# Kernel tuning notes

Hardware: AMD Instinct MI355X
Metric: run time of the kernel (lower is better)

The kernel has to match this reference:

```python
import jax, jax.numpy as jnp
import numpy as np

N_NODES = 200000
N_EDGES = 1000000
N_Q = 64
N_REL_ROWS = 401  # 2*n_rel + 1
D = 128
A = 64


def setup_inputs() -> dict:
    key = jax.random.key(0)
    ks = jax.random.split(key, 16)
    s = 0.05  # param scale
    return {
        'hidden': jax.random.normal(ks[0], (N_NODES, D), jnp.float32),
        'q_emb': jax.random.normal(ks[1], (N_Q, D), jnp.float32),
        'rela_embed': jax.random.normal(ks[2], (N_REL_ROWS, D), jnp.float32),
        'Ws_w': jax.random.normal(ks[3], (A, D), jnp.float32) * s,
        'Ws_b': jax.random.normal(ks[4], (A,), jnp.float32) * s,
        'Wr_w': jax.random.normal(ks[5], (A, D), jnp.float32) * s,
        'Wq_w': jax.random.normal(ks[6], (A, D), jnp.float32) * s,
        'Wqr_w': jax.random.normal(ks[7], (A, D), jnp.float32) * s,
        'walpha_w': jax.random.normal(ks[8], (1, A), jnp.float32) * s,
        'walpha_b': jax.random.normal(ks[9], (1,), jnp.float32) * s,
        'Wh_w': jax.random.normal(ks[10], (D, D), jnp.float32) * s,
        'r_idx': jax.random.randint(ks[11], (N_EDGES,), 0, N_Q, jnp.int32),
        'rel': jax.random.randint(ks[12], (N_EDGES,), 0, N_REL_ROWS, jnp.int32),
        'sub': jax.random.randint(ks[13], (N_EDGES,), 0, N_NODES, jnp.int32),
        'obj': jax.random.randint(ks[14], (N_EDGES,), 0, N_NODES, jnp.int32),
    }


def reference(hidden, q_emb, rela_embed, Ws_w, Ws_b, Wr_w, Wq_w, Wqr_w,
              walpha_w, walpha_b, Wh_w, r_idx, rel, sub, obj):
    # Gather per-edge features (memory-bound irregular access)
    hs = hidden[sub]          # [E, D]
    hr = rela_embed[rel]      # [E, D]
    h_qr = q_emb[r_idx]       # [E, D]

    # Fused small attention MLP: sigmoid(w_alpha(relu(Ws hs + Wr hr + Wq hq + Wqr (hr*hq))))
    pre = (jnp.einsum('ed,ad->ea', hs, Ws_w) + Ws_b
           + jnp.einsum('ed,ad->ea', hr, Wr_w)
           + jnp.einsum('ed,ad->ea', h_qr, Wq_w)
           + jnp.einsum('ed,ad->ea', hr * h_qr, Wqr_w))  # [E, A]
    alpha = jax.nn.sigmoid(jnp.einsum('ea,oa->eo', jax.nn.relu(pre), walpha_w) + walpha_b)  # [E, 1]

    # Gated message + scatter-sum aggregation per target node
    message = alpha * (hs * hr)                                   # [E, D]
    message_agg = jax.ops.segment_sum(message, obj, num_segments=N_NODES)  # [N, D]

    hidden_new = jax.nn.relu(jnp.einsum('nd,od->no', message_agg, Wh_w))   # [N, D]
    return hidden_new, alpha
```

## Files before the change

### kernel.cpp

```cpp
#include <hip/hip_runtime.h>
#include <hip/hip_bf16.h>
#include <hip/hip_fp8.h>

#define N_NODES 200000
#define N_EDGES 1000000
#define NQ 64
#define NRELR 401
#define DIM 128
#define AA 64
#define NBK 3125
#define CAP 512

typedef __attribute__((ext_vector_type(8))) short short8_t;
typedef __attribute__((ext_vector_type(4))) float f32x4;

static __device__ inline short f2bs(float f) {
  __hip_bfloat16 h = __float2bfloat16(f);
  return __builtin_bit_cast(short, h);
}
static __device__ inline float bs2f(unsigned short u) {
  unsigned x = ((unsigned)u) << 16;
  return __builtin_bit_cast(float, x);
}
static __device__ inline unsigned pk2(float lo, float hi) {
  unsigned short a = (unsigned short)__builtin_bit_cast(short, __float2bfloat16(lo));
  unsigned short b = (unsigned short)__builtin_bit_cast(short, __float2bfloat16(hi));
  return (unsigned)a | ((unsigned)b << 16);
}
static __device__ inline unsigned char f2e4(float f) {
  __hip_fp8_e4m3 h(f);
  return (unsigned char)h.__x;
}
static __device__ inline float e42f(unsigned char b) {
  __hip_fp8_e4m3 h;
  h.__x = (__hip_fp8_storage_t)b;
  return (float)h;
}
static __device__ inline void atomic_pk_bf16_s(unsigned voff, unsigned val,
                                               const unsigned short* base) {
  asm volatile("global_atomic_pk_add_bf16 %0, %1, %2"
               :: "v"(voff), "v"(val), "s"((unsigned long long)base) : "memory");
}
static __device__ inline short8_t pack8(float4 a, float4 b) {
  short8_t v;
  v[0] = f2bs(a.x); v[1] = f2bs(a.y); v[2] = f2bs(a.z); v[3] = f2bs(a.w);
  v[4] = f2bs(b.x); v[5] = f2bs(b.y); v[6] = f2bs(b.z); v[7] = f2bs(b.w);
  return v;
}

#define CBK 401
#define SBK 512
#define HBK 64
__global__ __launch_bounds__(256) void prep_kernel(
    const float* __restrict__ hidden, const float* __restrict__ qemb,
    const float* __restrict__ rela, const float* __restrict__ Ws,
    const float* __restrict__ Wsb, const float* __restrict__ Wr,
    const float* __restrict__ Wq, const float* __restrict__ Wqr,
    const int* __restrict__ obj,
    unsigned char* __restrict__ C8, unsigned char* __restrict__ S8,
    unsigned short* __restrict__ relab, short* __restrict__ hidb,
    int* __restrict__ cnt) {
  int b = blockIdx.x;
  int t = threadIdx.x;

  if (b < CBK) {
    __shared__ __hip_bfloat16 hqs[64][136];
    __shared__ __hip_bfloat16 vts[128][72];
    __shared__ float hr_f[128];
    __shared__ float trp[4][64];
    __shared__ float tr_s[64];
    int rho = b;

    if (t < 128) {
      float hv = rela[rho * DIM + t];
      hr_f[t] = hv;
      relab[rho * DIM + t] = (unsigned short)f2bs(hv);
    }
    __syncthreads();
    for (int i = t; i < 64 * 128; i += 256) {
      int q = i >> 7, d = i & 127;
      hqs[q][d] = __float2bfloat16(qemb[i]);
      int a = i >> 7;
      vts[d][a] = __float2bfloat16(Wq[i] + hr_f[d] * Wqr[i]);
    }
    {
      int a = t & 63, qt = t >> 6;
      const float* wr = Wr + a * DIM + qt * 32;
      float p = 0.f;
#pragma unroll 8
      for (int i = 0; i < 32; ++i) p += wr[i] * hr_f[qt * 32 + i];
      trp[qt][a] = p;
    }
    __syncthreads();
    if (t < 64)
      tr_s[t] = trp[0][t] + trp[1][t] + trp[2][t] + trp[3][t] + Wsb[t];
    __syncthreads();

    int qg = t >> 4, ag = t & 15;
    int q0 = qg * 4, a0 = ag * 4;
    float acc[4][4];
#pragma unroll
    for (int i = 0; i < 4; ++i)
#pragma unroll
      for (int j = 0; j < 4; ++j) acc[i][j] = 0.f;
    for (int d = 0; d < DIM; ++d) {
      float hv[4], wv[4];
#pragma unroll
      for (int i = 0; i < 4; ++i) hv[i] = __bfloat162float(hqs[q0 + i][d]);
#pragma unroll
      for (int j = 0; j < 4; ++j) wv[j] = __bfloat162float(vts[d][a0 + j]);
#pragma unroll
      for (int i = 0; i < 4; ++i)
#pragma unroll
        for (int j = 0; j < 4; ++j) acc[i][j] += hv[i] * wv[j];
    }
#pragma unroll
    for (int i = 0; i < 4; ++i)
#pragma unroll
      for (int j = 0; j < 4; ++j) {
        int q = q0 + i, a = a0 + j;
        C8[((size_t)rho * 64 + q) * 64 + a] = f2e4(acc[i][j] + tr_s[a]);
      }
  } else if (b < CBK + SBK) {
    int lane = t & 63;
    int lr = lane & 15, lg = lane >> 4;
    int gw = (b - CBK) * 4 + (t >> 6);
    const int NWV = SBK * 4;

    short8_t bf[4][4];
#pragma unroll
    for (int ot = 0; ot < 4; ++ot)
#pragma unroll
      for (int kt = 0; kt < 4; ++kt) {
        const float* wp = Ws + (size_t)(ot * 16 + lr) * DIM + kt * 32 + lg * 8;
        bf[ot][kt] = pack8(*(const float4*)wp, *(const float4*)(wp + 4));
      }

    for (int tt = gw; tt < N_NODES / 16; tt += NWV) {
      const float* ap = hidden + (size_t)tt * 16 * DIM + (size_t)lr * DIM;
      short8_t a[4];
#pragma unroll
      for (int kt = 0; kt < 4; ++kt) {
        const float* p = ap + kt * 32 + lg * 8;
        a[kt] = pack8(*(const float4*)p, *(const float4*)(p + 4));
        *(short8_t*)(hidb + ((size_t)tt * 16 + lr) * DIM + kt * 32 + lg * 8) = a[kt];
      }
      f32x4 acc[4];
#pragma unroll
      for (int ot = 0; ot < 4; ++ot) {
        acc[ot] = (f32x4){0.f, 0.f, 0.f, 0.f};
#pragma unroll
        for (int kt = 0; kt < 4; ++kt)
          acc[ot] = __builtin_amdgcn_mfma_f32_16x16x32_bf16(a[kt], bf[ot][kt], acc[ot], 0, 0, 0);
      }
#pragma unroll
      for (int ot = 0; ot < 4; ++ot)
#pragma unroll
        for (int r = 0; r < 4; ++r)
          S8[((size_t)tt * 16 + lg * 4 + r) * 64 + ot * 16 + lr] = f2e4(acc[ot][r]);
    }
  } else {
    __shared__ int h[NBK];
    int z = b - CBK - SBK;
    for (int i = t; i < NBK; i += 256) h[i] = 0;
    __syncthreads();
    for (int e = z * 256 + t; e < N_EDGES; e += HBK * 256)
      atomicAdd(&h[obj[e] >> 6], 1);
    __syncthreads();
    for (int i = t; i < NBK; i += 256)
      if (h[i]) atomicAdd(&cnt[i], h[i]);
  }
}

__global__ __launch_bounds__(256) void scan_kernel(
    const int* __restrict__ cnt, int* __restrict__ base, int* __restrict__ cur) {
  __shared__ int part[256];
  int t = threadIdx.x;
  const int PER = (NBK + 255) / 256;
  int lo = t * PER;
  int loc[PER];
  int s = 0;
#pragma unroll
  for (int k = 0; k < PER; ++k) {
    loc[k] = s;
    int idx = lo + k;
    s += (idx < NBK) ? cnt[idx] : 0;
  }
  part[t] = s;
  __syncthreads();
  for (int off = 1; off < 256; off <<= 1) {
    int v = (t >= off) ? part[t - off] : 0;
    __syncthreads();
    part[t] += v;
    __syncthreads();
  }
  int pre = (t == 0) ? 0 : part[t - 1];
#pragma unroll
  for (int k = 0; k < PER; ++k) {
    int idx = lo + k;
    if (idx < NBK) {
      base[idx] = pre + loc[k];
      cur[idx] = pre + loc[k];
    }
  }
  if (t == 255) base[NBK] = part[255];
}

__global__ __launch_bounds__(256) void scatter2_kernel(
    const int* __restrict__ ridx, const int* __restrict__ rel,
    const int* __restrict__ sub, const int* __restrict__ obj,
    int* __restrict__ cur, uint2* __restrict__ recs) {
  __shared__ int h[NBK];
  __shared__ int loff[NBK];
  __shared__ int lcur[NBK];
  int t = threadIdx.x, z = blockIdx.x;
  for (int i = t; i < NBK; i += 256) { h[i] = 0; lcur[i] = 0; }
  __syncthreads();
  for (int e = z * 256 + t; e < N_EDGES; e += HBK * 256)
    atomicAdd(&h[obj[e] >> 6], 1);
  __syncthreads();
  for (int i = t; i < NBK; i += 256)
    if (h[i]) loff[i] = atomicAdd(&cur[i], h[i]);
  __syncthreads();
  for (int e = z * 256 + t; e < N_EDGES; e += HBK * 256) {
    int s = sub[e], r = rel[e], q = ridx[e], o = obj[e];
    int bb = o >> 6;
    int rq = r * 64 + q;
    int p = loff[bb] + atomicAdd(&lcur[bb], 1);
    uint2 rc;
    rc.x = (unsigned)s | ((unsigned)(o & 63) << 18) | ((unsigned)(rq & 0xFF) << 24);
    rc.y = (unsigned)(rq >> 8) | ((unsigned)e << 7);
    recs[p] = rc;
  }
}

__global__ __launch_bounds__(256) void bucket2_kernel(
    const unsigned* __restrict__ hid32, const unsigned* __restrict__ rel32,
    const unsigned char* __restrict__ S8, const unsigned char* __restrict__ C8,
    const float* __restrict__ wal, const float* __restrict__ walb,
    const int* __restrict__ base, const uint2* __restrict__ recs,
    unsigned* __restrict__ agg32, float* __restrict__ alpha_out) {
  __shared__ uint2 lrec[CAP];
  __shared__ unsigned short ord[CAP];
  __shared__ int cnt2[64];
  __shared__ int scn[65];
  __shared__ int curs[64];
  int t = threadIdx.x, b = blockIdx.x;
  int lane = t & 63, w = t >> 6;
  int lo = base[b], hi = base[b + 1];
  int cnt = hi - lo;
  int nbase = b * 64;
  float wa = wal[lane];
  float wb = walb[0];

  if (t < 64) cnt2[t] = 0;
  __syncthreads();

  if (cnt <= CAP) {
    for (int i = t; i < cnt; i += 256) {
      uint2 rc = recs[lo + i];
      lrec[i] = rc;
      atomicAdd(&cnt2[(rc.x >> 18) & 63], 1);
    }
    __syncthreads();
    if (t < 64) scn[t + 1] = cnt2[t];
    if (t == 0) scn[0] = 0;
    __syncthreads();
    for (int off = 1; off < 64; off <<= 1) {
      int v = 0;
      if (t < 64) { v = scn[t + 1]; if (t + 1 > off) v += scn[t + 1 - off]; }
      __syncthreads();
      if (t < 64) scn[t + 1] = v;
      __syncthreads();
    }
    if (t < 64) curs[t] = scn[t];
    __syncthreads();
    for (int i = t; i < cnt; i += 256) {
      int oin = (lrec[i].x >> 18) & 63;
      int p = atomicAdd(&curs[oin], 1);
      ord[p] = (unsigned short)i;
    }
    __syncthreads();

    int n0 = w * 16;
    int s0 = scn[n0], s1 = scn[n0 + 16];
    float m0 = 0.f, m1 = 0.f;
    int curn = -1;
    for (int j = s0; j < s1; j += 4) {
      int nv = s1 - j;
      if (nv > 4) nv = 4;
      int sdx[4], on[4], rq[4], ei[4];
      float y[4], h0[4], h1[4], g0[4], g1[4];
#pragma unroll
      for (int u = 0; u < 4; ++u) {
        int idx = (u < nv) ? (j + u) : j;
        uint2 rc = lrec[ord[idx]];
        unsigned rx = __builtin_amdgcn_readfirstlane(rc.x);
        unsigned ry = __builtin_amdgcn_readfirstlane(rc.y);
        sdx[u] = rx & 0x3FFFF;
        on[u] = (rx >> 18) & 63;
        rq[u] = ((rx >> 24) & 0xFF) | ((ry & 0x7F) << 8);
        ei[u] = ry >> 7;
      }
#pragma unroll
      for (int u = 0; u < 4; ++u) {
        float x = e42f(S8[(size_t)sdx[u] * 64 + lane]) +
                  e42f(C8[(size_t)rq[u] * 64 + lane]);
        y[u] = fmaxf(x, 0.f) * wa;
      }
#pragma unroll
      for (int u = 0; u < 4; ++u) {
        unsigned hp = hid32[(size_t)sdx[u] * 64 + lane];
        unsigned rp = rel32[(size_t)(rq[u] >> 6) * 64 + lane];
        h0[u] = bs2f((unsigned short)(hp & 0xffff));
        h1[u] = bs2f((unsigned short)(hp >> 16));
        g0[u] = bs2f((unsigned short)(rp & 0xffff));
        g1[u] = bs2f((unsigned short)(rp >> 16));
      }
#pragma unroll
      for (int off = 32; off; off >>= 1) {
#pragma unroll
        for (int u = 0; u < 4; ++u) y[u] += __shfl_xor(y[u], off);
      }
#pragma unroll
      for (int u = 0; u < 4; ++u) {
        if (u < nv) {
          float al = 1.f / (1.f + __expf(-(y[u] + wb)));
          if (on[u] != curn) {
            if (curn >= 0)
              agg32[(size_t)(nbase + curn) * 64 + lane] = pk2(m0, m1);
            curn = on[u];
            m0 = 0.f; m1 = 0.f;
          }
          m0 += al * h0[u] * g0[u];
          m1 += al * h1[u] * g1[u];
          if (lane == 0) alpha_out[ei[u]] = al;
        }
      }
    }
    if (curn >= 0)
      agg32[(size_t)(nbase + curn) * 64 + lane] = pk2(m0, m1);
    for (int n = n0; n < n0 + 16; ++n) {
      if (cnt2[n] == 0)
        agg32[(size_t)(nbase + n) * 64 + lane] = 0u;
    }
  } else {
    for (int n = w; n < 64; n += 4)
      agg32[(size_t)(nbase + n) * 64 + lane] = 0u;
    __syncthreads();
    unsigned voff = (unsigned)lane * 4;
    for (int i = lo + w * 4; i < hi; i += 16) {
      int nv = hi - i;
      if (nv > 4) nv = 4;
      for (int u = 0; u < 4; ++u) {
        if (u >= nv) break;
        uint2 rc = recs[i + u];
        unsigned rx = __builtin_amdgcn_readfirstlane(rc.x);
        unsigned ry = __builtin_amdgcn_readfirstlane(rc.y);
        int sdx = rx & 0x3FFFF;
        int on = (rx >> 18) & 63;
        int rq = ((rx >> 24) & 0xFF) | ((ry & 0x7F) << 8);
        int ei = ry >> 7;
        float x = e42f(S8[(size_t)sdx * 64 + lane]) + e42f(C8[(size_t)rq * 64 + lane]);
        float y = fmaxf(x, 0.f) * wa;
        for (int off = 32; off; off >>= 1) y += __shfl_xor(y, off);
        float al = 1.f / (1.f + __expf(-(y + wb)));
        unsigned hp = hid32[(size_t)sdx * 64 + lane];
        unsigned rp = rel32[(size_t)(rq >> 6) * 64 + lane];
        float v0 = al * bs2f((unsigned short)(hp & 0xffff)) * bs2f((unsigned short)(rp & 0xffff));
        float v1 = al * bs2f((unsigned short)(hp >> 16)) * bs2f((unsigned short)(rp >> 16));
        atomic_pk_bf16_s(voff, pk2(v0, v1), (const unsigned short*)(agg32 + (size_t)(nbase + on) * 64));
        if (lane == 0) alpha_out[ei] = al;
      }
    }
  }
}

__global__ __launch_bounds__(256) void out_gemm_bf(
    const float* __restrict__ Wh, const short* __restrict__ aggb,
    float* __restrict__ out) {
  int lane = threadIdx.x & 63;
  int lr = lane & 15, lg = lane >> 4;
  int gw = (blockIdx.x * blockDim.x + threadIdx.x) >> 6;
  int nwv = (gridDim.x * blockDim.x) >> 6;

  short8_t b[8][4];
#pragma unroll
  for (int ot = 0; ot < 8; ++ot)
#pragma unroll
    for (int kt = 0; kt < 4; ++kt) {
      const float* wp = Wh + (size_t)(ot * 16 + lr) * DIM + kt * 32 + lg * 8;
      b[ot][kt] = pack8(*(const float4*)wp, *(const float4*)(wp + 4));
    }

  for (int t = gw; t < N_NODES / 16; t += nwv) {
    const short* ap = aggb + ((size_t)t * 16 + lr) * DIM;
    short8_t a[4];
#pragma unroll
    for (int kt = 0; kt < 4; ++kt)
      a[kt] = *(const short8_t*)(ap + kt * 32 + lg * 8);
    f32x4 acc[8];
#pragma unroll
    for (int ot = 0; ot < 8; ++ot) {
      acc[ot] = (f32x4){0.f, 0.f, 0.f, 0.f};
#pragma unroll
      for (int kt = 0; kt < 4; ++kt)
        acc[ot] = __builtin_amdgcn_mfma_f32_16x16x32_bf16(a[kt], b[ot][kt], acc[ot], 0, 0, 0);
    }
    float* op = out + (size_t)t * 16 * DIM;
#pragma unroll
    for (int ot = 0; ot < 8; ++ot)
#pragma unroll
      for (int r = 0; r < 4; ++r)
        op[(size_t)(lg * 4 + r) * DIM + ot * 16 + lr] = fmaxf(acc[ot][r], 0.f);
  }
}

__global__ __launch_bounds__(256) void tq_kernel(
    const float* __restrict__ qemb, const float* __restrict__ Wq,
    float* __restrict__ Tq) {
  int t = blockIdx.x * 256 + threadIdx.x;
  if (t >= NQ * AA) return;
  int q = t >> 6, a = t & 63;
  float s = 0.f;
#pragma unroll 4
  for (int d = 0; d < DIM; ++d) s += qemb[q * DIM + d] * Wq[a * DIM + d];
  Tq[t] = s;
}

__global__ __launch_bounds__(256) void build_C_old(
    const float* __restrict__ qemb, const float* __restrict__ rela,
    const float* __restrict__ Wr, const float* __restrict__ Wqr,
    const float* __restrict__ Wsb, const float* __restrict__ Tq,
    __hip_bfloat16* __restrict__ Cout) {
  __shared__ float hrq[64 * 129];
  __shared__ float wqrT[128 * 65];
  __shared__ float wrT[128 * 65];
  __shared__ float hr_s[128];
  __shared__ float tr_s[64];
  int rho = blockIdx.x;
  int t = threadIdx.x;
  if (t < 128) hr_s[t] = rela[rho * DIM + t];
  __syncthreads();
  for (int i = t; i < 64 * 128; i += 256) {
    int a = i >> 7, d = i & 127;
    hrq[a * 129 + d] = qemb[i] * hr_s[d];
    wqrT[d * 65 + a] = Wqr[i];
    wrT[d * 65 + a] = Wr[i];
  }
  __syncthreads();
  if (t < 64) {
    float s = 0.f;
#pragma unroll 4
    for (int d = 0; d < DIM; ++d) s += wrT[d * 65 + t] * hr_s[d];
    tr_s[t] = s + Wsb[t];
  }
  __syncthreads();
  int qg = t >> 4, ag = t & 15;
  int q0 = qg * 4, a0 = ag * 4;
  float acc[4][4];
#pragma unroll
  for (int i = 0; i < 4; ++i)
#pragma unroll
    for (int j = 0; j < 4; ++j) acc[i][j] = 0.f;
  for (int d = 0; d < DIM; ++d) {
    float hv[4], wv[4];
#pragma unroll
    for (int i = 0; i < 4; ++i) hv[i] = hrq[(q0 + i) * 129 + d];
#pragma unroll
    for (int j = 0; j < 4; ++j) wv[j] = wqrT[d * 65 + a0 + j];
#pragma unroll
    for (int i = 0; i < 4; ++i)
#pragma unroll
      for (int j = 0; j < 4; ++j) acc[i][j] += hv[i] * wv[j];
  }
#pragma unroll
  for (int i = 0; i < 4; ++i)
#pragma unroll
    for (int j = 0; j < 4; ++j) {
      int q = q0 + i, a = a0 + j;
      Cout[(rho * 64 + q) * 64 + a] = __float2bfloat16(acc[i][j] + Tq[q * 64 + a] + tr_s[a]);
    }
}

__global__ __launch_bounds__(256) void build_S_old(
    const float* __restrict__ hidden, const float* __restrict__ Ws,
    __hip_bfloat16* __restrict__ Sout) {
  int lane = threadIdx.x & 63;
  int lr = lane & 15, lg = lane >> 4;
  int gw = (blockIdx.x * blockDim.x + threadIdx.x) >> 6;
  int nwv = (gridDim.x * blockDim.x) >> 6;
  short8_t b[4][4];
#pragma unroll
  for (int ot = 0; ot < 4; ++ot)
#pragma unroll
    for (int kt = 0; kt < 4; ++kt) {
      const float* wp = Ws + (size_t)(ot * 16 + lr) * DIM + kt * 32 + lg * 8;
      b[ot][kt] = pack8(*(const float4*)wp, *(const float4*)(wp + 4));
    }
  for (int t = gw; t < N_NODES / 16; t += nwv) {
    const float* ap = hidden + (size_t)t * 16 * DIM + (size_t)lr * DIM;
    short8_t a[4];
#pragma unroll
    for (int kt = 0; kt < 4; ++kt) {
      const float* p = ap + kt * 32 + lg * 8;
      a[kt] = pack8(*(const float4*)p, *(const float4*)(p + 4));
    }
    f32x4 acc[4];
#pragma unroll
    for (int ot = 0; ot < 4; ++ot) {
      acc[ot] = (f32x4){0.f, 0.f, 0.f, 0.f};
#pragma unroll
      for (int kt = 0; kt < 4; ++kt)
        acc[ot] = __builtin_amdgcn_mfma_f32_16x16x32_bf16(a[kt], b[ot][kt], acc[ot], 0, 0, 0);
    }
#pragma unroll
    for (int ot = 0; ot < 4; ++ot)
#pragma unroll
      for (int r = 0; r < 4; ++r)
        Sout[((size_t)t * 16 + lg * 4 + r) * 64 + ot * 16 + lr] = __float2bfloat16(acc[ot][r]);
  }
}

__global__ __launch_bounds__(256) void edge_kernel_old(
    const float* __restrict__ hidden, const float* __restrict__ rela,
    const __hip_bfloat16* __restrict__ S, const __hip_bfloat16* __restrict__ C,
    const float* __restrict__ wal, const float* __restrict__ walb,
    const int* __restrict__ ridx, const int* __restrict__ rel,
    const int* __restrict__ sub, const int* __restrict__ obj,
    float* __restrict__ agg, float* __restrict__ alpha_out) {
  int lane = threadIdx.x & 63;
  int wid = (blockIdx.x * blockDim.x + threadIdx.x) >> 6;
  const int CH = 124;
  int e0 = wid * CH;
  if (e0 >= N_EDGES) return;
  int e1 = e0 + CH;
  if (e1 > N_EDGES) e1 = N_EDGES;
  float wa = wal[lane];
  float wb = walb[0];
  for (int e = e0; e < e1; e += 4) {
    int4 ss = *(const int4*)(sub + e);
    int4 rr = *(const int4*)(rel + e);
    int4 qq = *(const int4*)(ridx + e);
    int4 oo = *(const int4*)(obj + e);
    int s[4] = {ss.x, ss.y, ss.z, ss.w};
    int r[4] = {rr.x, rr.y, rr.z, rr.w};
    int q[4] = {qq.x, qq.y, qq.z, qq.w};
    int o[4] = {oo.x, oo.y, oo.z, oo.w};
    float y[4];
#pragma unroll
    for (int u = 0; u < 4; ++u) {
      float x = __bfloat162float(S[(size_t)s[u] * 64 + lane]) +
                __bfloat162float(C[((size_t)r[u] * 64 + q[u]) * 64 + lane]);
      y[u] = fmaxf(x, 0.f) * wa;
    }
    float h0[4], h1[4], r0[4], r1[4];
#pragma unroll
    for (int u = 0; u < 4; ++u) {
      h0[u] = hidden[(size_t)s[u] * DIM + lane];
      h1[u] = hidden[(size_t)s[u] * DIM + 64 + lane];
      r0[u] = rela[(size_t)r[u] * DIM + lane];
      r1[u] = rela[(size_t)r[u] * DIM + 64 + lane];
    }
#pragma unroll
    for (int off = 32; off; off >>= 1) {
#pragma unroll
      for (int u = 0; u < 4; ++u) y[u] += __shfl_xor(y[u], off);
    }
    float al[4];
#pragma unroll
    for (int u = 0; u < 4; ++u) al[u] = 1.f / (1.f + __expf(-(y[u] + wb)));
#pragma unroll
    for (int u = 0; u < 4; ++u) {
      unsafeAtomicAdd(&agg[(size_t)o[u] * DIM + lane], al[u] * h0[u] * r0[u]);
      unsafeAtomicAdd(&agg[(size_t)o[u] * DIM + 64 + lane], al[u] * h1[u] * r1[u]);
    }
    if (lane == 0)
      *(float4*)(alpha_out + e) = make_float4(al[0], al[1], al[2], al[3]);
  }
}

__global__ __launch_bounds__(256) void out_gemm_old(
    const float* __restrict__ Wh, float* __restrict__ agg) {
  int lane = threadIdx.x & 63;
  int lr = lane & 15, lg = lane >> 4;
  int gw = (blockIdx.x * blockDim.x + threadIdx.x) >> 6;
  int nwv = (gridDim.x * blockDim.x) >> 6;
  short8_t b[8][4];
#pragma unroll
  for (int ot = 0; ot < 8; ++ot)
#pragma unroll
    for (int kt = 0; kt < 4; ++kt) {
      const float* wp = Wh + (size_t)(ot * 16 + lr) * DIM + kt * 32 + lg * 8;
      b[ot][kt] = pack8(*(const float4*)wp, *(const float4*)(wp + 4));
    }
  for (int t = gw; t < N_NODES / 16; t += nwv) {
    float* ap = agg + (size_t)t * 16 * DIM + (size_t)lr * DIM;
    short8_t a[4];
#pragma unroll
    for (int kt = 0; kt < 4; ++kt) {
      const float* p = ap + kt * 32 + lg * 8;
      a[kt] = pack8(*(const float4*)p, *(const float4*)(p + 4));
    }
    f32x4 acc[8];
#pragma unroll
    for (int ot = 0; ot < 8; ++ot) {
      acc[ot] = (f32x4){0.f, 0.f, 0.f, 0.f};
#pragma unroll
      for (int kt = 0; kt < 4; ++kt)
        acc[ot] = __builtin_amdgcn_mfma_f32_16x16x32_bf16(a[kt], b[ot][kt], acc[ot], 0, 0, 0);
    }
    float* op = agg + (size_t)t * 16 * DIM;
#pragma unroll
    for (int ot = 0; ot < 8; ++ot)
#pragma unroll
      for (int r = 0; r < 4; ++r)
        op[(size_t)(lg * 4 + r) * DIM + ot * 16 + lr] = fmaxf(acc[ot][r], 0.f);
  }
}

extern "C" void kernel_launch(void* const* d_in, const int* in_sizes, int n_in,
                              void* d_out, int out_size, void* d_ws, size_t ws_size,
                              hipStream_t stream) {
  const float* hidden = (const float*)d_in[0];
  const float* qemb   = (const float*)d_in[1];
  const float* rela   = (const float*)d_in[2];
  const float* Ws_w   = (const float*)d_in[3];
  const float* Ws_b   = (const float*)d_in[4];
  const float* Wr_w   = (const float*)d_in[5];
  const float* Wq_w   = (const float*)d_in[6];
  const float* Wqr_w  = (const float*)d_in[7];
  const float* wal_w  = (const float*)d_in[8];
  const float* wal_b  = (const float*)d_in[9];
  const float* Wh_w   = (const float*)d_in[10];
  const int* r_idx    = (const int*)d_in[11];
  const int* rel      = (const int*)d_in[12];
  const int* sub      = (const int*)d_in[13];
  const int* obj      = (const int*)d_in[14];

  float* out_hidden = (float*)d_out;
  float* out_alpha  = out_hidden + (size_t)N_NODES * DIM;

  char* ws = (char*)d_ws;
  const size_t OFF_C8  = 0;
  const size_t SZ_C8   = (size_t)NRELR * 64 * 64;
  const size_t OFF_S8  = OFF_C8 + SZ_C8;
  const size_t SZ_S8   = (size_t)N_NODES * 64;
  const size_t OFF_RB  = OFF_S8 + SZ_S8;
  const size_t SZ_RB   = (size_t)NRELR * DIM * 2;
  const size_t OFF_HB  = OFF_RB + SZ_RB;
  const size_t SZ_HB   = (size_t)N_NODES * DIM * 2;
  const size_t OFF_AG  = OFF_HB + SZ_HB;
  const size_t OFF_CNT = OFF_AG + SZ_HB;
  const size_t OFF_BASE= OFF_CNT + 16384;
  const size_t OFF_CUR = OFF_BASE + 16384;
  const size_t OFF_REC = OFF_CUR + 16384;
  const size_t FULL_NEED = OFF_REC + (size_t)N_EDGES * 8;

  if (ws_size >= FULL_NEED) {
    unsigned char* C8 = (unsigned char*)(ws + OFF_C8);
    unsigned char* S8 = (unsigned char*)(ws + OFF_S8);
    unsigned short* relab = (unsigned short*)(ws + OFF_RB);
    short* hidb = (short*)(ws + OFF_HB);
    unsigned short* aggb = (unsigned short*)(ws + OFF_AG);
    int* cnt  = (int*)(ws + OFF_CNT);
    int* base = (int*)(ws + OFF_BASE);
    int* cur  = (int*)(ws + OFF_CUR);
    uint2* recs = (uint2*)(ws + OFF_REC);

    hipMemsetAsync(cnt, 0, (size_t)NBK * 4, stream);
    prep_kernel<<<CBK + SBK + HBK, 256, 0, stream>>>(
        hidden, qemb, rela, Ws_w, Ws_b, Wr_w, Wq_w, Wqr_w, obj,
        C8, S8, relab, hidb, cnt);
    scan_kernel<<<1, 256, 0, stream>>>(cnt, base, cur);
    scatter2_kernel<<<HBK, 256, 0, stream>>>(r_idx, rel, sub, obj, cur, recs);
    bucket2_kernel<<<NBK, 256, 0, stream>>>(
        (const unsigned*)hidb, (const unsigned*)relab, S8, C8,
        wal_w, wal_b, base, recs, (unsigned*)aggb, out_alpha);
    out_gemm_bf<<<512, 256, 0, stream>>>(Wh_w, (const short*)aggb, out_hidden);
  } else {
    const size_t OFF_CBo = 16384;
    const size_t SZ_CBo  = (size_t)NRELR * 64 * 64 * 2;
    const size_t OFF_SBo = OFF_CBo + SZ_CBo;
    float* Tq = (float*)ws;
    __hip_bfloat16* Cb = (__hip_bfloat16*)(ws + OFF_CBo);
    __hip_bfloat16* Sb = (__hip_bfloat16*)(ws + OFF_SBo);
    hipMemsetAsync(out_hidden, 0, (size_t)N_NODES * DIM * sizeof(float), stream);
    tq_kernel<<<16, 256, 0, stream>>>(qemb, Wq_w, Tq);
    build_C_old<<<NRELR, 256, 0, stream>>>(qemb, rela, Wr_w, Wqr_w, Ws_b, Tq, Cb);
    build_S_old<<<512, 256, 0, stream>>>(hidden, Ws_w, Sb);
    edge_kernel_old<<<2048, 256, 0, stream>>>(hidden, rela, Sb, Cb, wal_w, wal_b,
                                              r_idx, rel, sub, obj, out_hidden, out_alpha);
    out_gemm_old<<<512, 256, 0, stream>>>(Wh_w, out_hidden);
  }
}
```

Before: 304.5 us.

## Replace atomic bucket counting with per-block histograms and deterministic offsets

The histogram blocks now write a per-block 2D histogram instead of doing global atomics, and a new column-wise prefix kernel computes per-block offsets and totals. The scatter kernel no longer recounts its histogram and no longer does global atomics; it reads precomputed offsets. The number of histogram and scatter blocks rises from 64 to 256 (or 128, depending on workspace size) to expose more parallelism in the counting sort. This costs one extra small kernel launch and extra workspace traffic for the 2D histogram.

```diff
diff --git a/kernel.cpp b/kernel.cpp
--- a/kernel.cpp
+++ b/kernel.cpp
@@ -50,7 +50,6 @@
 
 #define CBK 401
 #define SBK 512
-#define HBK 64
 __global__ __launch_bounds__(256) void prep_kernel(
     const float* __restrict__ hidden, const float* __restrict__ qemb,
     const float* __restrict__ rela, const float* __restrict__ Ws,
@@ -59,7 +58,7 @@
     const int* __restrict__ obj,
     unsigned char* __restrict__ C8, unsigned char* __restrict__ S8,
     unsigned short* __restrict__ relab, short* __restrict__ hidb,
-    int* __restrict__ cnt) {
+    int* __restrict__ hist2d, int znum) {
   int b = blockIdx.x;
   int t = threadIdx.x;
 
@@ -164,16 +163,30 @@
     int z = b - CBK - SBK;
     for (int i = t; i < NBK; i += 256) h[i] = 0;
     __syncthreads();
-    for (int e = z * 256 + t; e < N_EDGES; e += HBK * 256)
+    for (int e = z * 256 + t; e < N_EDGES; e += znum * 256)
       atomicAdd(&h[obj[e] >> 6], 1);
     __syncthreads();
     for (int i = t; i < NBK; i += 256)
-      if (h[i]) atomicAdd(&cnt[i], h[i]);
-  }
+      hist2d[(size_t)z * NBK + i] = h[i];
+  }
+}
+
+__global__ __launch_bounds__(256) void offsetsA_kernel(
+    const int* __restrict__ hist2d, int* __restrict__ off2d,
+    int* __restrict__ totals, int znum) {
+  int b0 = blockIdx.x * 256 + threadIdx.x;
+  if (b0 >= NBK) return;
+  int run = 0;
+  for (int z = 0; z < znum; ++z) {
+    int v = hist2d[(size_t)z * NBK + b0];
+    off2d[(size_t)z * NBK + b0] = run;
+    run += v;
+  }
+  totals[b0] = run;
 }
 
 __global__ __launch_bounds__(256) void scan_kernel(
-    const int* __restrict__ cnt, int* __restrict__ base, int* __restrict__ cur) {
+    const int* __restrict__ totals, int* __restrict__ base) {
   __shared__ int part[256];
   int t = threadIdx.x;
   const int PER = (NBK + 255) / 256;
@@ -184,7 +197,7 @@
   for (int k = 0; k < PER; ++k) {
     loc[k] = s;
     int idx = lo + k;
-    s += (idx < NBK) ? cnt[idx] : 0;
+    s += (idx < NBK) ? totals[idx] : 0;
   }
   part[t] = s;
   __syncthreads();
@@ -198,31 +211,25 @@
 #pragma unroll
   for (int k = 0; k < PER; ++k) {
     int idx = lo + k;
-    if (idx < NBK) {
-      base[idx] = pre + loc[k];
-      cur[idx] = pre + loc[k];
-    }
+    if (idx < NBK) base[idx] = pre + loc[k];
   }
   if (t == 255) base[NBK] = part[255];
 }
 
-__global__ __launch_bounds__(256) void scatter2_kernel(
+__global__ __launch_bounds__(256) void scatter3_kernel(
     const int* __restrict__ ridx, const int* __restrict__ rel,
     const int* __restrict__ sub, const int* __restrict__ obj,
-    int* __restrict__ cur, uint2* __restrict__ recs) {
-  __shared__ int h[NBK];
+    const int* __restrict__ base, const int* __restrict__ off2d,
+    uint2* __restrict__ recs, int znum) {
   __shared__ int loff[NBK];
   __shared__ int lcur[NBK];
   int t = threadIdx.x, z = blockIdx.x;
-  for (int i = t; i < NBK; i += 256) { h[i] = 0; lcur[i] = 0; }
+  for (int i = t; i < NBK; i += 256) {
+    loff[i] = base[i] + off2d[(size_t)z * NBK + i];
+    lcur[i] = 0;
+  }
   __syncthreads();
-  for (int e = z * 256 + t; e < N_EDGES; e += HBK * 256)
-    atomicAdd(&h[obj[e] >> 6], 1);
-  __syncthreads();
-  for (int i = t; i < NBK; i += 256)
-    if (h[i]) loff[i] = atomicAdd(&cur[i], h[i]);
-  __syncthreads();
-  for (int e = z * 256 + t; e < N_EDGES; e += HBK * 256) {
+  for (int e = z * 256 + t; e < N_EDGES; e += znum * 256) {
     int s = sub[e], r = rel[e], q = ridx[e], o = obj[e];
     int bb = o >> 6;
     int rq = r * 64 + q;
@@ -651,29 +658,41 @@
   const size_t OFF_HB  = OFF_RB + SZ_RB;
   const size_t SZ_HB   = (size_t)N_NODES * DIM * 2;
   const size_t OFF_AG  = OFF_HB + SZ_HB;
-  const size_t OFF_CNT = OFF_AG + SZ_HB;
-  const size_t OFF_BASE= OFF_CNT + 16384;
-  const size_t OFF_CUR = OFF_BASE + 16384;
-  const size_t OFF_REC = OFF_CUR + 16384;
-  const size_t FULL_NEED = OFF_REC + (size_t)N_EDGES * 8;
-
-  if (ws_size >= FULL_NEED) {
+  const size_t OFF_H2D = OFF_AG + SZ_HB;
+
+  int znum = 0;
+  size_t off_o2d = 0, off_tot = 0, off_base = 0, off_rec = 0;
+  for (int zc = 256; zc >= 128; zc >>= 1) {
+    size_t szh = (size_t)zc * NBK * 4;
+    size_t o2d = OFF_H2D + szh;
+    size_t tot = o2d + szh;
+    size_t bas = tot + 16384;
+    size_t rec = bas + 16384;
+    size_t need = rec + (size_t)N_EDGES * 8;
+    if (ws_size >= need) {
+      znum = zc; off_o2d = o2d; off_tot = tot; off_base = bas; off_rec = rec;
+      break;
+    }
+  }
+
+  if (znum) {
     unsigned char* C8 = (unsigned char*)(ws + OFF_C8);
     unsigned char* S8 = (unsigned char*)(ws + OFF_S8);
     unsigned short* relab = (unsigned short*)(ws + OFF_RB);
     short* hidb = (short*)(ws + OFF_HB);
     unsigned short* aggb = (unsigned short*)(ws + OFF_AG);
-    int* cnt  = (int*)(ws + OFF_CNT);
-    int* base = (int*)(ws + OFF_BASE);
-    int* cur  = (int*)(ws + OFF_CUR);
-    uint2* recs = (uint2*)(ws + OFF_REC);
-
-    hipMemsetAsync(cnt, 0, (size_t)NBK * 4, stream);
-    prep_kernel<<<CBK + SBK + HBK, 256, 0, stream>>>(
+    int* hist2d = (int*)(ws + OFF_H2D);
+    int* off2d  = (int*)(ws + off_o2d);
+    int* totals = (int*)(ws + off_tot);
+    int* base   = (int*)(ws + off_base);
+    uint2* recs = (uint2*)(ws + off_rec);
+
+    prep_kernel<<<CBK + SBK + znum, 256, 0, stream>>>(
         hidden, qemb, rela, Ws_w, Ws_b, Wr_w, Wq_w, Wqr_w, obj,
-        C8, S8, relab, hidb, cnt);
-    scan_kernel<<<1, 256, 0, stream>>>(cnt, base, cur);
-    scatter2_kernel<<<HBK, 256, 0, stream>>>(r_idx, rel, sub, obj, cur, recs);
+        C8, S8, relab, hidb, hist2d, znum);
+    offsetsA_kernel<<<(NBK + 255) / 256, 256, 0, stream>>>(hist2d, off2d, totals, znum);
+    scan_kernel<<<1, 256, 0, stream>>>(totals, base);
+    scatter3_kernel<<<znum, 256, 0, stream>>>(r_idx, rel, sub, obj, base, off2d, recs, znum);
     bucket2_kernel<<<NBK, 256, 0, stream>>>(
         (const unsigned*)hidb, (const unsigned*)relab, S8, C8,
         wal_w, wal_b, base, recs, (unsigned*)aggb, out_alpha);
```

After: 305.6 us. No clear change (+0.4%).
